# Kernel optimization log

Measured on AMD Instinct MI355X. Metric: run time of the kernel, lower is better.

## Reference

```python
import jax, jax.numpy as jnp
import numpy as np

TEMPERATURE = 0.5
NEG_INF = -1e9  # used to mask self-similarity diagonal before logsumexp


def setup_inputs() -> dict:
    key = jax.random.key(0)
    k1, k2 = jax.random.split(key)
    N, Z = 4096, 128
    z1 = jax.random.normal(k1, (N, Z), dtype=jnp.float32)
    z2 = jax.random.normal(k2, (N, Z), dtype=jnp.float32)
    return {"z1": z1, "z2": z2}


def reference(z1, z2):
    # NT-Xent (SimCLR) loss. Faithful to:
    #   sim = cosine_similarity over all pairs of concat([z1, z2])
    #   positives = sim diagonals at offsets +-N; negatives = all off-(self)diag entries
    #   cross_entropy with the positive as class 0  ->  -pos/T + logsumexp(all non-self sims / T)
    N = z1.shape[0]
    reps = jnp.concatenate([z1, z2], axis=0)                      # [2N, Z]
    # row-normalize once; cosine sim matrix is then a single GEMM
    norms = jnp.linalg.norm(reps, axis=-1, keepdims=True)
    # torch cosine_similarity clamps norms by eps=1e-8
    nreps = reps / jnp.maximum(norms, 1e-8)
    sim = nreps @ nreps.T                                          # [2N, 2N]
    # positives: sim[i, i+N] for i<N and sim[i, i-N] for i>=N
    l_pos = jnp.diagonal(sim, offset=N)                            # [N]
    r_pos = jnp.diagonal(sim, offset=-N)                           # [N]
    positives = jnp.concatenate([l_pos, r_pos])                    # [2N]
    # logsumexp over all entries except the self-similarity diagonal.
    # (The positive entry stays in the denominator exactly once, matching
    #  concat([positive, negatives]) in the original.)
    two_n = 2 * N
    self_mask = jnp.eye(two_n, dtype=bool)
    logits = jnp.where(self_mask, NEG_INF, sim / TEMPERATURE)      # [2N, 2N]
    lse = jax.nn.logsumexp(logits, axis=1)                         # [2N]
    per_row = lse - positives / TEMPERATURE                        # CE with label 0
    return jnp.sum(per_row) / two_n
```

## Files before the change

### kernel.cpp

```cpp
#include <hip/hip_runtime.h>
#include <hip/hip_bf16.h>


#define N_PAIRS 4096
#define ZDIM    128
#define NROWS   8192
#define QS 1.6986437717f

typedef __bf16 bf16x8 __attribute__((ext_vector_type(8)));
typedef float  floatx4 __attribute__((ext_vector_type(4)));

__global__ __launch_bounds__(256) void k_normalize(
    const float* __restrict__ z1, const float* __restrict__ z2,
    __hip_bfloat16* __restrict__ pack, float* __restrict__ pos,
    float* __restrict__ denom)
{
    const int zi = blockIdx.x * 256 + threadIdx.x;
    if (zi < NROWS) denom[zi] = 0.0f;

    const int w = threadIdx.x >> 6;
    const int lane = threadIdx.x & 63;
    const int p = blockIdx.x * 4 + w;
    const float2 a = ((const float2*)(z1 + (size_t)p * ZDIM))[lane];
    const float2 b = ((const float2*)(z2 + (size_t)p * ZDIM))[lane];
    float s1 = a.x * a.x + a.y * a.y;
    float s2 = b.x * b.x + b.y * b.y;
    float d  = a.x * b.x + a.y * b.y;
    #pragma unroll
    for (int off = 1; off < 64; off <<= 1) {
        s1 += __shfl_xor(s1, off, 64);
        s2 += __shfl_xor(s2, off, 64);
        d  += __shfl_xor(d,  off, 64);
    }
    const float n1 = fmaxf(sqrtf(s1), 1e-8f);
    const float n2 = fmaxf(sqrtf(s2), 1e-8f);
    const float i1 = 1.0f / n1, i2 = 1.0f / n2;
    const float q1 = i1 * QS, q2 = i2 * QS;
    float2 na; na.x = a.x * q1; na.y = a.y * q1;
    float2 nb; nb.x = b.x * q2; nb.y = b.y * q2;

    const int ks = lane >> 4;
    const int qq = (lane >> 2) & 3;
    const int jj = (lane & 3) * 2;
    const int r1 = p, r2 = p + N_PAIRS;
    const size_t i1e = ((size_t)((r1 >> 4) * 4 + ks)) * 512 + qq * 128 + (r1 & 15) * 8 + jj;
    const size_t i2e = ((size_t)((r2 >> 4) * 4 + ks)) * 512 + qq * 128 + (r2 & 15) * 8 + jj;
    *(__hip_bfloat162*)(pack + i1e) = __float22bfloat162_rn(na);
    *(__hip_bfloat162*)(pack + i2e) = __float22bfloat162_rn(nb);
    if (lane == 0) pos[p] = d * i1 * i2;
}

__global__ __launch_bounds__(256) void k_simsum(
    const __hip_bfloat16* __restrict__ pack, float* __restrict__ denom)
{
    const int tid  = threadIdx.x;
    const int lane = tid & 63;
    const int w    = tid >> 6;
    const int rt   = blockIdx.x >> 4;
    const int cs   = blockIdx.x & 15;
    const int q    = lane >> 4;
    const int l16  = lane & 15;

    const int rowb = rt * 256 + w * 64;
    const __hip_bfloat16* Abase =
        pack + ((size_t)(rowb >> 4) * 4) * 512 + lane * 8;
    bf16x8 afrag[4][4];
    #pragma unroll
    for (int mt = 0; mt < 4; ++mt)
        #pragma unroll
        for (int ks = 0; ks < 4; ++ks)
            afrag[mt][ks] = *(const bf16x8*)(Abase + mt * 2048 + ks * 512);

    float rowsum[4][4];
    #pragma unroll
    for (int mt = 0; mt < 4; ++mt)
        #pragma unroll
        for (int r = 0; r < 4; ++r) rowsum[mt][r] = 0.0f;

    const __hip_bfloat16* Bcol0 =
        pack + ((size_t)((cs * 512) >> 4) * 4) * 512 + lane * 8;

    auto loadB = [&](bf16x8 (&buf)[4][2], int hs) {
        const __hip_bfloat16* bp = Bcol0 + (size_t)hs * 4096;
        #pragma unroll
        for (int ks = 0; ks < 4; ++ks)
            #pragma unroll
            for (int nt = 0; nt < 2; ++nt)
                buf[ks][nt] = *(const bf16x8*)(bp + nt * 2048 + ks * 512);
    };

    auto compute = [&](bf16x8 (&buf)[4][2], int hs) {
        floatx4 acc[4][2];
        #pragma unroll
        for (int mt = 0; mt < 4; ++mt)
            #pragma unroll
            for (int nt = 0; nt < 2; ++nt) {
                acc[mt][nt].x = 0.f; acc[mt][nt].y = 0.f;
                acc[mt][nt].z = 0.f; acc[mt][nt].w = 0.f;
            }
        #pragma unroll
        for (int ks = 0; ks < 4; ++ks)
            #pragma unroll
            for (int mt = 0; mt < 4; ++mt)
                #pragma unroll
                for (int nt = 0; nt < 2; ++nt)
                    acc[mt][nt] = __builtin_amdgcn_mfma_f32_16x16x32_bf16(
                        afrag[mt][ks], buf[ks][nt], acc[mt][nt], 0, 0, 0);
        const int colb = cs * 512 + hs * 32;
        #pragma unroll
        for (int mt = 0; mt < 4; ++mt) {
            const int rowtb = rowb + mt * 16;
            #pragma unroll
            for (int nt = 0; nt < 2; ++nt) {
                const int coltb = colb + nt * 16;
                if (rowtb == coltb) {
                    #pragma unroll
                    for (int r = 0; r < 4; ++r) {
                        const float e = __builtin_amdgcn_exp2f(acc[mt][nt][r]);
                        rowsum[mt][r] += (l16 == q * 4 + r) ? 0.0f : e;
                    }
                } else {
                    #pragma unroll
                    for (int r = 0; r < 4; ++r)
                        rowsum[mt][r] += __builtin_amdgcn_exp2f(acc[mt][nt][r]);
                }
            }
        }
    };

    bf16x8 bufA[4][2], bufB[4][2];
    loadB(bufA, 0);
    for (int hs = 0; hs < 16; hs += 2) {
        loadB(bufB, hs + 1);
        compute(bufA, hs);
        loadB(bufA, (hs + 2) & 15);
        compute(bufB, hs + 1);
    }

    #pragma unroll
    for (int mt = 0; mt < 4; ++mt)
        #pragma unroll
        for (int r = 0; r < 4; ++r) {
            float s = rowsum[mt][r];
            s += __shfl_xor(s, 1, 64);
            s += __shfl_xor(s, 2, 64);
            s += __shfl_xor(s, 4, 64);
            s += __shfl_xor(s, 8, 64);
            rowsum[mt][r] = s;
        }
    if (l16 == 0) {
        #pragma unroll
        for (int mt = 0; mt < 4; ++mt)
            #pragma unroll
            for (int r = 0; r < 4; ++r) {
                const int grow = rowb + mt * 16 + q * 4 + r;
                atomicAdd(&denom[grow], rowsum[mt][r]);
            }
    }
}

__global__ __launch_bounds__(1024) void k_finish(
    const float* __restrict__ denom, const float* __restrict__ pos,
    float* __restrict__ out)
{
    __shared__ float red[16];
    const int t = threadIdx.x;
    const int lane = t & 63, wv = t >> 6;
    float s = 0.0f;
    for (int i = t; i < NROWS; i += 1024) s += __logf(denom[i]);
    float p = 0.0f;
    for (int i = t; i < N_PAIRS; i += 1024) p += pos[i];
    float v = s - 4.0f * p;
    #pragma unroll
    for (int off = 1; off < 64; off <<= 1) v += __shfl_xor(v, off, 64);
    if (lane == 0) red[wv] = v;
    __syncthreads();
    if (wv == 0) {
        float x = (lane < 16) ? red[lane] : 0.0f;
        #pragma unroll
        for (int off = 1; off < 16; off <<= 1) x += __shfl_xor(x, off, 64);
        if (lane == 0) out[0] = x / (float)NROWS;
    }
}

extern "C" void kernel_launch(void* const* d_in, const int* in_sizes, int n_in,
                              void* d_out, int out_size, void* d_ws, size_t ws_size,
                              hipStream_t stream) {
    const float* z1 = (const float*)d_in[0];
    const float* z2 = (const float*)d_in[1];
    float* out = (float*)d_out;

    char* ws = (char*)d_ws;
    __hip_bfloat16* pack = (__hip_bfloat16*)ws;
    float* denom = (float*)(ws + (size_t)NROWS * ZDIM * 2);
    float* pos   = denom + NROWS;

    k_normalize<<<N_PAIRS / 4, 256, 0, stream>>>(z1, z2, pack, pos, denom);
    k_simsum<<<512, 256, 0, stream>>>(pack, denom);
    k_finish<<<1, 1024, 0, stream>>>(denom, pos, out);
}
```

Baseline: 83.40 us.

## Switch similarity GEMM from bf16 to fp8 MFMA with repacked layout

Normalized rows are now quantized to fp8 instead of bf16, and the pack layout is reorganized for 16x16x32 fp8 MFMA operands. This halves the operand bytes and uses the higher-throughput fp8 matrix path. The grid doubles to 1024 blocks with half the columns each, and the explicit B-fragment double buffering is dropped. Fp8 quantization of logits scaled by 1/(T·ln2) adds numerical error to the exp-sum, which may affect tolerance.

```diff
diff --git a/kernel.cpp b/kernel.cpp
--- a/kernel.cpp
+++ b/kernel.cpp
@@ -7,12 +7,12 @@
 #define NROWS   8192
 #define QS 1.6986437717f
 
-typedef __bf16 bf16x8 __attribute__((ext_vector_type(8)));
-typedef float  floatx4 __attribute__((ext_vector_type(4)));
+typedef float floatx4 __attribute__((ext_vector_type(4)));
+typedef long  longx2  __attribute__((ext_vector_type(2)));
 
 __global__ __launch_bounds__(256) void k_normalize(
     const float* __restrict__ z1, const float* __restrict__ z2,
-    __hip_bfloat16* __restrict__ pack, float* __restrict__ pos,
+    char* __restrict__ pack, float* __restrict__ pos,
     float* __restrict__ denom)
 {
     const int zi = blockIdx.x * 256 + threadIdx.x;
@@ -36,40 +36,42 @@
     const float n2 = fmaxf(sqrtf(s2), 1e-8f);
     const float i1 = 1.0f / n1, i2 = 1.0f / n2;
     const float q1 = i1 * QS, q2 = i2 * QS;
-    float2 na; na.x = a.x * q1; na.y = a.y * q1;
-    float2 nb; nb.x = b.x * q2; nb.y = b.y * q2;
-
-    const int ks = lane >> 4;
-    const int qq = (lane >> 2) & 3;
-    const int jj = (lane & 3) * 2;
+
+    const int ks2  = lane >> 5;
+    const int half = (lane >> 4) & 1;
+    const int qq   = (lane >> 2) & 3;
+    const int jj   = (lane & 3) * 2;
     const int r1 = p, r2 = p + N_PAIRS;
-    const size_t i1e = ((size_t)((r1 >> 4) * 4 + ks)) * 512 + qq * 128 + (r1 & 15) * 8 + jj;
-    const size_t i2e = ((size_t)((r2 >> 4) * 4 + ks)) * 512 + qq * 128 + (r2 & 15) * 8 + jj;
-    *(__hip_bfloat162*)(pack + i1e) = __float22bfloat162_rn(na);
-    *(__hip_bfloat162*)(pack + i2e) = __float22bfloat162_rn(nb);
+    const size_t o1 = ((size_t)((r1 >> 4) * 2 + ks2)) * 1024 + qq * 256
+                    + (r1 & 15) * 16 + half * 8 + jj;
+    const size_t o2 = ((size_t)((r2 >> 4) * 2 + ks2)) * 1024 + qq * 256
+                    + (r2 & 15) * 16 + half * 8 + jj;
+    const int pk1 = __builtin_amdgcn_cvt_pk_fp8_f32(a.x * q1, a.y * q1, 0, false);
+    const int pk2 = __builtin_amdgcn_cvt_pk_fp8_f32(b.x * q2, b.y * q2, 0, false);
+    *(unsigned short*)(pack + o1) = (unsigned short)pk1;
+    *(unsigned short*)(pack + o2) = (unsigned short)pk2;
     if (lane == 0) pos[p] = d * i1 * i2;
 }
 
 __global__ __launch_bounds__(256) void k_simsum(
-    const __hip_bfloat16* __restrict__ pack, float* __restrict__ denom)
+    const char* __restrict__ pack, float* __restrict__ denom)
 {
     const int tid  = threadIdx.x;
     const int lane = tid & 63;
     const int w    = tid >> 6;
-    const int rt   = blockIdx.x >> 4;
-    const int cs   = blockIdx.x & 15;
+    const int rt   = blockIdx.x >> 5;
+    const int cs   = blockIdx.x & 31;
     const int q    = lane >> 4;
     const int l16  = lane & 15;
 
     const int rowb = rt * 256 + w * 64;
-    const __hip_bfloat16* Abase =
-        pack + ((size_t)(rowb >> 4) * 4) * 512 + lane * 8;
-    bf16x8 afrag[4][4];
+    const char* Abase = pack + (size_t)(rowb >> 4) * 2048 + lane * 16;
+    longx2 afrag[4][2];
     #pragma unroll
     for (int mt = 0; mt < 4; ++mt)
         #pragma unroll
-        for (int ks = 0; ks < 4; ++ks)
-            afrag[mt][ks] = *(const bf16x8*)(Abase + mt * 2048 + ks * 512);
+        for (int ks2 = 0; ks2 < 2; ++ks2)
+            afrag[mt][ks2] = *(const longx2*)(Abase + mt * 2048 + ks2 * 1024);
 
     float rowsum[4][4];
     #pragma unroll
@@ -77,19 +79,17 @@
         #pragma unroll
         for (int r = 0; r < 4; ++r) rowsum[mt][r] = 0.0f;
 
-    const __hip_bfloat16* Bcol0 =
-        pack + ((size_t)((cs * 512) >> 4) * 4) * 512 + lane * 8;
-
-    auto loadB = [&](bf16x8 (&buf)[4][2], int hs) {
-        const __hip_bfloat16* bp = Bcol0 + (size_t)hs * 4096;
-        #pragma unroll
-        for (int ks = 0; ks < 4; ++ks)
+    const char* Bcol0 = pack + (size_t)(cs * 16) * 2048 + lane * 16;
+
+    for (int hs = 0; hs < 8; ++hs) {
+        longx2 bfrag[2][2];
+        const char* bp = Bcol0 + (size_t)hs * 4096;
+        #pragma unroll
+        for (int ks2 = 0; ks2 < 2; ++ks2)
             #pragma unroll
             for (int nt = 0; nt < 2; ++nt)
-                buf[ks][nt] = *(const bf16x8*)(bp + nt * 2048 + ks * 512);
-    };
-
-    auto compute = [&](bf16x8 (&buf)[4][2], int hs) {
+                bfrag[nt][ks2] = *(const longx2*)(bp + nt * 2048 + ks2 * 1024);
+
         floatx4 acc[4][2];
         #pragma unroll
         for (int mt = 0; mt < 4; ++mt)
@@ -99,14 +99,22 @@
                 acc[mt][nt].z = 0.f; acc[mt][nt].w = 0.f;
             }
         #pragma unroll
-        for (int ks = 0; ks < 4; ++ks)
+        for (int ks2 = 0; ks2 < 2; ++ks2) {
             #pragma unroll
             for (int mt = 0; mt < 4; ++mt)
                 #pragma unroll
                 for (int nt = 0; nt < 2; ++nt)
-                    acc[mt][nt] = __builtin_amdgcn_mfma_f32_16x16x32_bf16(
-                        afrag[mt][ks], buf[ks][nt], acc[mt][nt], 0, 0, 0);
-        const int colb = cs * 512 + hs * 32;
+                    acc[mt][nt] = __builtin_amdgcn_mfma_f32_16x16x32_fp8_fp8(
+                        afrag[mt][ks2].x, bfrag[nt][ks2].x, acc[mt][nt], 0, 0, 0);
+            #pragma unroll
+            for (int mt = 0; mt < 4; ++mt)
+                #pragma unroll
+                for (int nt = 0; nt < 2; ++nt)
+                    acc[mt][nt] = __builtin_amdgcn_mfma_f32_16x16x32_fp8_fp8(
+                        afrag[mt][ks2].y, bfrag[nt][ks2].y, acc[mt][nt], 0, 0, 0);
+        }
+
+        const int colb = cs * 256 + hs * 32;
         #pragma unroll
         for (int mt = 0; mt < 4; ++mt) {
             const int rowtb = rowb + mt * 16;
@@ -126,15 +134,6 @@
                 }
             }
         }
-    };
-
-    bf16x8 bufA[4][2], bufB[4][2];
-    loadB(bufA, 0);
-    for (int hs = 0; hs < 16; hs += 2) {
-        loadB(bufB, hs + 1);
-        compute(bufA, hs);
-        loadB(bufA, (hs + 2) & 15);
-        compute(bufB, hs + 1);
     }
 
     #pragma unroll
@@ -191,11 +190,11 @@
     float* out = (float*)d_out;
 
     char* ws = (char*)d_ws;
-    __hip_bfloat16* pack = (__hip_bfloat16*)ws;
-    float* denom = (float*)(ws + (size_t)NROWS * ZDIM * 2);
+    char* pack = ws;
+    float* denom = (float*)(ws + (size_t)NROWS * ZDIM);
     float* pos   = denom + NROWS;
 
     k_normalize<<<N_PAIRS / 4, 256, 0, stream>>>(z1, z2, pack, pos, denom);
-    k_simsum<<<512, 256, 0, stream>>>(pack, denom);
+    k_simsum<<<1024, 256, 0, stream>>>(pack, denom);
     k_finish<<<1, 1024, 0, stream>>>(denom, pos, out);
 }
```

After: 95.66 us. 14.7% more time.

## Split column range across twice as many blocks and overlap exp epilogue with MFMA

Applied to the files above, without the earlier changes.

The similarity-sum kernel now launches 1024 blocks, each covering 256 columns instead of 512, and processes one 16-column tile per step instead of two. The loop is restructured so the exp/rowsum epilogue of the previous tile is interleaved with the load and MFMA of the next, aiming to overlap transcendental work with matrix ops and raise occupancy through lower register use. In exchange, each block reloads its A fragments for half the work, atomic traffic to the denominators doubles, and with a single buffer the loads are less deeply prefetched.

```diff
diff --git a/kernel.cpp b/kernel.cpp
--- a/kernel.cpp
+++ b/kernel.cpp
@@ -56,8 +56,8 @@
     const int tid  = threadIdx.x;
     const int lane = tid & 63;
     const int w    = tid >> 6;
-    const int rt   = blockIdx.x >> 4;
-    const int cs   = blockIdx.x & 15;
+    const int rt   = blockIdx.x >> 5;
+    const int cs   = blockIdx.x & 31;
     const int q    = lane >> 4;
     const int l16  = lane & 15;
 
@@ -78,64 +78,56 @@
         for (int r = 0; r < 4; ++r) rowsum[mt][r] = 0.0f;
 
     const __hip_bfloat16* Bcol0 =
-        pack + ((size_t)((cs * 512) >> 4) * 4) * 512 + lane * 8;
+        pack + ((size_t)(cs * 16) * 4) * 512 + lane * 8;
 
-    auto loadB = [&](bf16x8 (&buf)[4][2], int hs) {
-        const __hip_bfloat16* bp = Bcol0 + (size_t)hs * 4096;
+    bf16x8  bfrag[4];
+    floatx4 acc[4];
+
+    auto loadB = [&](int g) {
+        const __hip_bfloat16* bp = Bcol0 + (size_t)g * 2048;
         #pragma unroll
         for (int ks = 0; ks < 4; ++ks)
-            #pragma unroll
-            for (int nt = 0; nt < 2; ++nt)
-                buf[ks][nt] = *(const bf16x8*)(bp + nt * 2048 + ks * 512);
+            bfrag[ks] = *(const bf16x8*)(bp + ks * 512);
     };
-
-    auto compute = [&](bf16x8 (&buf)[4][2], int hs) {
-        floatx4 acc[4][2];
+    auto mfma_step = [&]() {
         #pragma unroll
-        for (int mt = 0; mt < 4; ++mt)
-            #pragma unroll
-            for (int nt = 0; nt < 2; ++nt) {
-                acc[mt][nt].x = 0.f; acc[mt][nt].y = 0.f;
-                acc[mt][nt].z = 0.f; acc[mt][nt].w = 0.f;
-            }
+        for (int mt = 0; mt < 4; ++mt) {
+            acc[mt].x = 0.f; acc[mt].y = 0.f; acc[mt].z = 0.f; acc[mt].w = 0.f;
+        }
         #pragma unroll
         for (int ks = 0; ks < 4; ++ks)
             #pragma unroll
             for (int mt = 0; mt < 4; ++mt)
-                #pragma unroll
-                for (int nt = 0; nt < 2; ++nt)
-                    acc[mt][nt] = __builtin_amdgcn_mfma_f32_16x16x32_bf16(
-                        afrag[mt][ks], buf[ks][nt], acc[mt][nt], 0, 0, 0);
-        const int colb = cs * 512 + hs * 32;
+                acc[mt] = __builtin_amdgcn_mfma_f32_16x16x32_bf16(
+                    afrag[mt][ks], bfrag[ks], acc[mt], 0, 0, 0);
+    };
+    auto epi = [&](int g) {
+        const int colb = cs * 256 + g * 16;
         #pragma unroll
         for (int mt = 0; mt < 4; ++mt) {
             const int rowtb = rowb + mt * 16;
-            #pragma unroll
-            for (int nt = 0; nt < 2; ++nt) {
-                const int coltb = colb + nt * 16;
-                if (rowtb == coltb) {
-                    #pragma unroll
-                    for (int r = 0; r < 4; ++r) {
-                        const float e = __builtin_amdgcn_exp2f(acc[mt][nt][r]);
-                        rowsum[mt][r] += (l16 == q * 4 + r) ? 0.0f : e;
-                    }
-                } else {
-                    #pragma unroll
-                    for (int r = 0; r < 4; ++r)
-                        rowsum[mt][r] += __builtin_amdgcn_exp2f(acc[mt][nt][r]);
+            if (rowtb == colb) {
+                #pragma unroll
+                for (int r = 0; r < 4; ++r) {
+                    const float e = __builtin_amdgcn_exp2f(acc[mt][r]);
+                    rowsum[mt][r] += (l16 == q * 4 + r) ? 0.0f : e;
                 }
+            } else {
+                #pragma unroll
+                for (int r = 0; r < 4; ++r)
+                    rowsum[mt][r] += __builtin_amdgcn_exp2f(acc[mt][r]);
             }
         }
     };
 
-    bf16x8 bufA[4][2], bufB[4][2];
-    loadB(bufA, 0);
-    for (int hs = 0; hs < 16; hs += 2) {
-        loadB(bufB, hs + 1);
-        compute(bufA, hs);
-        loadB(bufA, (hs + 2) & 15);
-        compute(bufB, hs + 1);
+    loadB(0);
+    mfma_step();
+    for (int g = 1; g < 16; ++g) {
+        loadB(g);
+        epi(g - 1);
+        mfma_step();
     }
+    epi(15);
 
     #pragma unroll
     for (int mt = 0; mt < 4; ++mt)
@@ -196,6 +188,6 @@
     float* pos   = denom + NROWS;
 
     k_normalize<<<N_PAIRS / 4, 256, 0, stream>>>(z1, z2, pack, pos, denom);
-    k_simsum<<<512, 256, 0, stream>>>(pack, denom);
+    k_simsum<<<1024, 256, 0, stream>>>(pack, denom);
     k_finish<<<1, 1024, 0, stream>>>(denom, pos, out);
 }
```

After: 90.33 us. +8.3%, slower.

## Stage shared B tiles in LDS via async global_load_lds across waves

Applied to the files above, without the earlier changes.

Previously each of the four waves in a block loaded the same B column fragments from global memory into registers. Now the block cooperatively stages each 64-column B slab into a double-buffered LDS area with global_load_lds, and every wave reads its fragments from LDS. This cuts redundant global/L2 traffic for B by roughly the wave count. The cost is a block-wide barrier per slab and extra LDS reads, which may limit overlap between loads and MFMA/exp work.

```diff
diff --git a/kernel.cpp b/kernel.cpp
--- a/kernel.cpp
+++ b/kernel.cpp
@@ -9,6 +9,9 @@
 
 typedef __bf16 bf16x8 __attribute__((ext_vector_type(8)));
 typedef float  floatx4 __attribute__((ext_vector_type(4)));
+typedef unsigned int u32;
+typedef __attribute__((address_space(3))) u32 lds_u32;
+typedef __attribute__((address_space(1))) const u32 glb_u32;
 
 __global__ __launch_bounds__(256) void k_normalize(
     const float* __restrict__ z1, const float* __restrict__ z2,
@@ -53,6 +56,8 @@
 __global__ __launch_bounds__(256) void k_simsum(
     const __hip_bfloat16* __restrict__ pack, float* __restrict__ denom)
 {
+    __shared__ char ldsB[2][16384];
+
     const int tid  = threadIdx.x;
     const int lane = tid & 63;
     const int w    = tid >> 6;
@@ -62,14 +67,13 @@
     const int l16  = lane & 15;
 
     const int rowb = rt * 256 + w * 64;
-    const __hip_bfloat16* Abase =
-        pack + ((size_t)(rowb >> 4) * 4) * 512 + lane * 8;
+    const char* Abase = (const char*)pack + (size_t)(rowb >> 4) * 4096 + lane * 16;
     bf16x8 afrag[4][4];
     #pragma unroll
     for (int mt = 0; mt < 4; ++mt)
         #pragma unroll
         for (int ks = 0; ks < 4; ++ks)
-            afrag[mt][ks] = *(const bf16x8*)(Abase + mt * 2048 + ks * 512);
+            afrag[mt][ks] = *(const bf16x8*)(Abase + mt * 4096 + ks * 1024);
 
     float rowsum[4][4];
     #pragma unroll
@@ -77,19 +81,29 @@
         #pragma unroll
         for (int r = 0; r < 4; ++r) rowsum[mt][r] = 0.0f;
 
-    const __hip_bfloat16* Bcol0 =
-        pack + ((size_t)((cs * 512) >> 4) * 4) * 512 + lane * 8;
-
-    auto loadB = [&](bf16x8 (&buf)[4][2], int hs) {
-        const __hip_bfloat16* bp = Bcol0 + (size_t)hs * 4096;
+    const char* Bsrc = (const char*)pack + (size_t)cs * 131072;
+
+    auto stage = [&](int g, int b) {
+        const char* src = Bsrc + (size_t)g * 16384;
+        #pragma unroll
+        for (int c = 0; c < 4; ++c) {
+            const int chunk = w * 4 + c;
+            __builtin_amdgcn_global_load_lds(
+                (glb_u32*)(src + chunk * 1024 + lane * 16),
+                (lds_u32*)(&ldsB[b][chunk * 1024]),
+                16, 0, 0);
+        }
+    };
+
+    auto substep = [&](int g, int b, int s) {
+        bf16x8 bfrag[4][2];
         #pragma unroll
         for (int ks = 0; ks < 4; ++ks)
             #pragma unroll
             for (int nt = 0; nt < 2; ++nt)
-                buf[ks][nt] = *(const bf16x8*)(bp + nt * 2048 + ks * 512);
-    };
-
-    auto compute = [&](bf16x8 (&buf)[4][2], int hs) {
+                bfrag[ks][nt] = *(const bf16x8*)
+                    (&ldsB[b][((2 * s + nt) * 4 + ks) * 1024 + lane * 16]);
+
         floatx4 acc[4][2];
         #pragma unroll
         for (int mt = 0; mt < 4; ++mt)
@@ -105,8 +119,9 @@
                 #pragma unroll
                 for (int nt = 0; nt < 2; ++nt)
                     acc[mt][nt] = __builtin_amdgcn_mfma_f32_16x16x32_bf16(
-                        afrag[mt][ks], buf[ks][nt], acc[mt][nt], 0, 0, 0);
-        const int colb = cs * 512 + hs * 32;
+                        afrag[mt][ks], bfrag[ks][nt], acc[mt][nt], 0, 0, 0);
+
+        const int colb = cs * 512 + g * 64 + s * 32;
         #pragma unroll
         for (int mt = 0; mt < 4; ++mt) {
             const int rowtb = rowb + mt * 16;
@@ -128,13 +143,13 @@
         }
     };
 
-    bf16x8 bufA[4][2], bufB[4][2];
-    loadB(bufA, 0);
-    for (int hs = 0; hs < 16; hs += 2) {
-        loadB(bufB, hs + 1);
-        compute(bufA, hs);
-        loadB(bufA, (hs + 2) & 15);
-        compute(bufB, hs + 1);
+    stage(0, 0);
+    __syncthreads();
+    for (int g = 0; g < 8; ++g) {
+        if (g < 7) stage(g + 1, (g + 1) & 1);
+        substep(g, g & 1, 0);
+        substep(g, g & 1, 1);
+        __syncthreads();
     }
 
     #pragma unroll
```

Result: slower. 114.1 us (+36.8%).
